# Performance work log

Measured on AMD Instinct MI355X. Metric: run time of the kernel, lower is better.

The kernel has to match this reference:

```python
import jax, jax.numpy as jnp
import numpy as np

N_NODES = 100000
N_EDGES = 1200000
N_GRAPHS = 1024
IN_DIM, HIDDEN, OUT_DIM = 4, 64, 2
BN_EPS = 1e-5


def setup_inputs() -> dict:
    key = jax.random.key(0)
    ks = jax.random.split(key, 12)
    x = jax.random.normal(ks[0], (N_NODES, IN_DIM), dtype=jnp.float32)
    edge_index = jax.random.randint(ks[1], (2, N_EDGES), 0, N_NODES, dtype=jnp.int64)
    batch = jnp.sort(jax.random.randint(ks[2], (N_NODES,), 0, N_GRAPHS, dtype=jnp.int64))
    s = 1.0 / np.sqrt(HIDDEN)
    return {
        "x": x,
        "edge_index": edge_index,
        "batch": batch,
        "W_enc": jax.random.normal(ks[3], (IN_DIM, HIDDEN), dtype=jnp.float32) * 0.5,
        "b_enc": jnp.zeros((HIDDEN,), dtype=jnp.float32),
        "bn_gamma": jnp.ones((HIDDEN,), dtype=jnp.float32),
        "bn_beta": jnp.zeros((HIDDEN,), dtype=jnp.float32),
        "bn_mean": jax.random.normal(ks[4], (HIDDEN,), dtype=jnp.float32) * 0.1,
        "bn_var": jax.random.uniform(ks[5], (HIDDEN,), dtype=jnp.float32, minval=0.5, maxval=1.5),
        "W_gcn": jax.random.normal(ks[6], (HIDDEN, HIDDEN), dtype=jnp.float32) * s,
        "b_gcn": jnp.zeros((HIDDEN,), dtype=jnp.float32),
        "W_cls1": jax.random.normal(ks[7], (HIDDEN, HIDDEN), dtype=jnp.float32) * s,
        "b_cls1": jnp.zeros((HIDDEN,), dtype=jnp.float32),
        "W_cls2": jax.random.normal(ks[8], (HIDDEN, OUT_DIM), dtype=jnp.float32) * s,
        "b_cls2": jnp.zeros((OUT_DIM,), dtype=jnp.float32),
    }


def reference(x, edge_index, batch, W_enc, b_enc, bn_gamma, bn_beta, bn_mean, bn_var,
              W_gcn, b_gcn, W_cls1, b_cls1, W_cls2, b_cls2):
    n = x.shape[0]
    # Encoder: Linear -> ReLU -> Dropout(eval=identity) -> BatchNorm1d (running stats)
    h = jnp.maximum(x @ W_enc + b_enc, 0.0)
    h = (h - bn_mean) * jax.lax.rsqrt(bn_var + BN_EPS) * bn_gamma + bn_beta
    # GCNConv (PyG): add self-loops, symmetric deg^{-1/2} normalization
    loop = jnp.arange(n, dtype=edge_index.dtype)
    src = jnp.concatenate([edge_index[0], loop])  # [E+N]
    dst = jnp.concatenate([edge_index[1], loop])
    deg = jnp.zeros((n,), dtype=h.dtype).at[dst].add(1.0)
    dis = jnp.where(deg > 0, jax.lax.rsqrt(jnp.maximum(deg, 1.0)), 0.0)
    norm = dis[src] * dis[dst]  # [E+N]
    hw = h @ W_gcn  # [N, H]
    msg = hw[src] * norm[:, None]  # gather + scale, [E+N, H]
    agg = jax.ops.segment_sum(msg, dst, num_segments=n) + b_gcn
    agg = jnp.maximum(agg, 0.0)  # .relu()
    # global_mean_pool over graphs
    sums = jax.ops.segment_sum(agg, batch, num_segments=N_GRAPHS)  # [G, H]
    cnts = jax.ops.segment_sum(jnp.ones((n,), dtype=agg.dtype), batch, num_segments=N_GRAPHS)
    gm = sums / jnp.maximum(cnts, 1.0)[:, None]
    # Classifier: Linear -> ReLU -> Dropout(eval) -> Linear
    out = jnp.maximum(gm @ W_cls1 + b_cls1, 0.0) @ W_cls2 + b_cls2
    return out
```

## Files before the change

kernel.cpp:

```cpp
#include <hip/hip_runtime.h>

#define N_NODES  100000
#define N_EDGES  1200000
#define N_GRAPHS 1024

#define BUCK_SHIFT 10
#define BUCK_NODES 1024
#define NBUCK 98
#define FBLK  512
#define CHUNK ((N_EDGES + FBLK - 1) / FBLK)

__device__ __forceinline__ unsigned short f2bf(float f) {
  unsigned u = __float_as_uint(f);
  return (unsigned short)((u + 0x7fffu + ((u >> 16) & 1u)) >> 16);
}
__device__ __forceinline__ float bf2f(unsigned short b) {
  return __uint_as_float(((unsigned)b) << 16);
}

__global__ __launch_bounds__(256) void k_cnt(const int* __restrict__ ei,
                                             int* __restrict__ cnt,
                                             float* __restrict__ gsum) {
  __shared__ int h[NBUCK];
  int t = threadIdx.x;
  for (int i = t; i < NBUCK; i += 256) h[i] = 0;
  int gi = blockIdx.x * 256 + t;
  if (gi < N_GRAPHS * 64) gsum[gi] = 0.f;
  __syncthreads();
  int start = blockIdx.x * CHUNK, end = min(start + CHUNK, N_EDGES);
  for (int e = start + t; e < end; e += 256)
    atomicAdd(&h[ei[N_EDGES + e] >> BUCK_SHIFT], 1);
  __syncthreads();
  for (int b = t; b < NBUCK; b += 256)
    cnt[b * FBLK + blockIdx.x] = h[b];
}

__global__ __launch_bounds__(256) void k_colscan(int* __restrict__ cnt,
                                                 int* __restrict__ tot) {
  __shared__ int wsum[4];
  int b = blockIdx.x, t = threadIdx.x;
  int v0 = cnt[b * FBLK + 2 * t], v1 = cnt[b * FBLK + 2 * t + 1];
  int a = v0 + v1;
  int lane = t & 63, w = t >> 6;
  int incl = a;
  #pragma unroll
  for (int off = 1; off < 64; off <<= 1) {
    int y = __shfl_up(incl, off);
    if (lane >= off) incl += y;
  }
  if (lane == 63) wsum[w] = incl;
  __syncthreads();
  if (t == 0) {
    int s = 0;
    #pragma unroll
    for (int i = 0; i < 4; ++i) { int x = wsum[i]; wsum[i] = s; s += x; }
    tot[b] = s;
  }
  __syncthreads();
  int excl = wsum[w] + incl - a;
  cnt[b * FBLK + 2 * t] = excl;
  cnt[b * FBLK + 2 * t + 1] = excl + v0;
}

__global__ __launch_bounds__(256) void k_fill(const int* __restrict__ ei,
                                              const int* __restrict__ cnt,
                                              const int* __restrict__ tot,
                                              int* __restrict__ binned) {
  __shared__ int totS[NBUCK];
  __shared__ int cur[NBUCK];
  int t = threadIdx.x, blk = blockIdx.x;
  if (t < NBUCK) totS[t] = tot[t];
  __syncthreads();
  if (t < NBUCK) {
    int s = 0;
    for (int i = 0; i < t; ++i) s += totS[i];
    cur[t] = s + cnt[t * FBLK + blk];
  }
  __syncthreads();
  int start = blk * CHUNK, end = min(start + CHUNK, N_EDGES);
  for (int e = start + t; e < end; e += 256) {
    int src = ei[e];
    int dst = ei[N_EDGES + e];
    int b = dst >> BUCK_SHIFT;
    int p = atomicAdd(&cur[b], 1);
    binned[p] = src | ((dst & (BUCK_NODES - 1)) << 17);
  }
}

__global__ __launch_bounds__(1024) void k_csr(const int* __restrict__ tot,
                                              const int* __restrict__ binned,
                                              int* __restrict__ csr,
                                              int* __restrict__ row_start,
                                              float* __restrict__ dis) {
  __shared__ int hist[BUCK_NODES];
  __shared__ int wsum[16];
  __shared__ int b0S;
  int t = threadIdx.x;
  int blk = blockIdx.x;
  int lane = t & 63, w = t >> 6;
  int pv = (t < blk) ? tot[t] : 0;
  #pragma unroll
  for (int off = 32; off > 0; off >>= 1) pv += __shfl_down(pv, off);
  if (lane == 0) wsum[w] = pv;
  hist[t] = 0;
  __syncthreads();
  if (t == 0) {
    int s = 0;
    #pragma unroll
    for (int i = 0; i < 16; ++i) s += wsum[i];
    b0S = s;
  }
  __syncthreads();
  int b0 = b0S;
  int nE = tot[blk];
  int node0 = blk << BUCK_SHIFT;
  int nNodes = min(BUCK_NODES, N_NODES - node0);
  for (int i = t; i < nE; i += 1024)
    atomicAdd(&hist[(unsigned)binned[b0 + i] >> 17], 1);
  __syncthreads();
  int v = hist[t];
  int incl = v;
  #pragma unroll
  for (int off = 1; off < 64; off <<= 1) {
    int y = __shfl_up(incl, off);
    if (lane >= off) incl += y;
  }
  if (lane == 63) wsum[w] = incl;
  __syncthreads();
  if (t == 0) {
    int s = 0;
    #pragma unroll
    for (int i = 0; i < 16; ++i) { int x = wsum[i]; wsum[i] = s; s += x; }
  }
  __syncthreads();
  int excl = wsum[w] + incl - v;
  hist[t] = excl;
  if (t < nNodes) {
    row_start[node0 + t] = b0 + excl;
    dis[node0 + t] = rsqrtf((float)(v + 1));
  }
  if (t == 0 && blk == NBUCK - 1) row_start[N_NODES] = N_EDGES;
  __syncthreads();
  for (int i = t; i < nE; i += 1024) {
    int vv = binned[b0 + i];
    int d = (unsigned)vv >> 17;
    int p = atomicAdd(&hist[d], 1);
    csr[b0 + p] = vv & 0x1FFFF;
  }
}

__global__ __launch_bounds__(256) void k_enc(
    const float* __restrict__ x,
    const float* __restrict__ Wenc, const float* __restrict__ benc,
    const float* __restrict__ gamma, const float* __restrict__ beta,
    const float* __restrict__ mean,  const float* __restrict__ var,
    const float* __restrict__ Wgcn,  const float* __restrict__ dis,
    unsigned short* __restrict__ hws) {
  int lane = threadIdx.x & 63;
  int wv = (blockIdx.x * 256 + threadIdx.x) >> 6;
  float be = benc[lane];
  float sc = gamma[lane] * rsqrtf(var[lane] + 1e-5f);
  float mu = mean[lane], bt = beta[lane];
  float w0 = Wenc[lane], w1 = Wenc[64 + lane], w2 = Wenc[128 + lane], w3 = Wenc[192 + lane];
  float wreg[64];
  #pragma unroll
  for (int k = 0; k < 64; ++k) wreg[k] = Wgcn[k * 64 + lane];
  int n0 = wv * 16;
  for (int i = 0; i < 16; ++i) {
    int n = n0 + i;
    float4 xv = ((const float4*)x)[n];
    float h = fmaf(xv.w, w3, fmaf(xv.z, w2, fmaf(xv.y, w1, fmaf(xv.x, w0, be))));
    h = fmaxf(h, 0.f);
    float hbn = (h - mu) * sc + bt;
    int hb = __float_as_int(hbn);
    float a0 = 0.f, a1 = 0.f, a2 = 0.f, a3 = 0.f;
    #pragma unroll
    for (int k = 0; k < 64; k += 4) {
      a0 = fmaf(__int_as_float(__builtin_amdgcn_readlane(hb, k)),     wreg[k],     a0);
      a1 = fmaf(__int_as_float(__builtin_amdgcn_readlane(hb, k + 1)), wreg[k + 1], a1);
      a2 = fmaf(__int_as_float(__builtin_amdgcn_readlane(hb, k + 2)), wreg[k + 2], a2);
      a3 = fmaf(__int_as_float(__builtin_amdgcn_readlane(hb, k + 3)), wreg[k + 3], a3);
    }
    float acc = ((a0 + a1) + (a2 + a3)) * dis[n];
    hws[(size_t)n * 64 + lane] = f2bf(acc);
  }
}

__global__ __launch_bounds__(64) void k_gather(
    const int* __restrict__ row_start, const int* __restrict__ csr,
    const float* __restrict__ dis, const unsigned short* __restrict__ hws,
    const int* __restrict__ batch, const float* __restrict__ bgcn,
    float* __restrict__ gsum) {
  int lane = threadIdx.x;
  int nb = blockIdx.x * 4;
  float bias = bgcn[lane];
  float vout[4];
  int gid[4];
  #pragma unroll
  for (int k = 0; k < 4; ++k) {
    int n = nb + k;
    int st = row_start[n], en = row_start[n + 1];
    float dn = dis[n];
    float a0 = 0.f, a1 = 0.f, a2 = 0.f, a3 = 0.f;
    for (int c = st; c < en; c += 64) {
      int m = min(64, en - c);
      int chunk = (c + lane < en) ? csr[c + lane] : 0;
      int j = 0;
      for (; j + 4 <= m; j += 4) {
        int s0 = __builtin_amdgcn_readlane(chunk, j);
        int s1 = __builtin_amdgcn_readlane(chunk, j + 1);
        int s2 = __builtin_amdgcn_readlane(chunk, j + 2);
        int s3 = __builtin_amdgcn_readlane(chunk, j + 3);
        a0 += bf2f(hws[(size_t)s0 * 64 + lane]);
        a1 += bf2f(hws[(size_t)s1 * 64 + lane]);
        a2 += bf2f(hws[(size_t)s2 * 64 + lane]);
        a3 += bf2f(hws[(size_t)s3 * 64 + lane]);
      }
      for (; j < m; ++j) {
        int s = __builtin_amdgcn_readlane(chunk, j);
        a0 += bf2f(hws[(size_t)s * 64 + lane]);
      }
    }
    float self = bf2f(hws[(size_t)n * 64 + lane]);
    vout[k] = fmaxf(dn * (((a0 + a1) + (a2 + a3)) + self) + bias, 0.f);
    gid[k] = batch[n];
  }
  float vs = vout[0];
  int cg = gid[0];
  #pragma unroll
  for (int k = 1; k < 4; ++k) {
    if (gid[k] == cg) vs += vout[k];
    else {
      atomicAdd(&gsum[cg * 64 + lane], vs);
      vs = vout[k]; cg = gid[k];
    }
  }
  atomicAdd(&gsum[cg * 64 + lane], vs);
}

__global__ void k_cls(const float* __restrict__ gsum, const int* __restrict__ batch,
                      const float* __restrict__ W1, const float* __restrict__ b1,
                      const float* __restrict__ W2, const float* __restrict__ b2,
                      float* __restrict__ out) {
  __shared__ float gm[64];
  __shared__ int cntS;
  int j = threadIdx.x;
  int g = blockIdx.x;
  if (j == 0) {
    int lo = 0, hi = N_NODES;
    while (lo < hi) { int mid = (lo + hi) >> 1; if (batch[mid] < g) lo = mid + 1; else hi = mid; }
    int lo2 = lo, hi2 = N_NODES;
    while (lo2 < hi2) { int mid = (lo2 + hi2) >> 1; if (batch[mid] < g + 1) lo2 = mid + 1; else hi2 = mid; }
    cntS = lo2 - lo;
  }
  __syncthreads();
  float denom = fmaxf((float)cntS, 1.0f);
  gm[j] = gsum[g * 64 + j] / denom;
  __syncthreads();
  float hid = b1[j];
  #pragma unroll
  for (int k = 0; k < 64; ++k) hid += gm[k] * W1[k * 64 + j];
  hid = fmaxf(hid, 0.f);
  float o0 = hid * W2[j * 2 + 0];
  float o1 = hid * W2[j * 2 + 1];
  #pragma unroll
  for (int off = 32; off > 0; off >>= 1) {
    o0 += __shfl_down(o0, off);
    o1 += __shfl_down(o1, off);
  }
  if (j == 0) {
    out[g * 2 + 0] = o0 + b2[0];
    out[g * 2 + 1] = o1 + b2[1];
  }
}

extern "C" void kernel_launch(void* const* d_in, const int* in_sizes, int n_in,
                              void* d_out, int out_size, void* d_ws, size_t ws_size,
                              hipStream_t stream) {
  const float* x     = (const float*)d_in[0];
  const int*   ei    = (const int*)d_in[1];
  const int*   batch = (const int*)d_in[2];
  const float* Wenc  = (const float*)d_in[3];
  const float* benc  = (const float*)d_in[4];
  const float* gamma = (const float*)d_in[5];
  const float* beta  = (const float*)d_in[6];
  const float* mean  = (const float*)d_in[7];
  const float* var   = (const float*)d_in[8];
  const float* Wgcn  = (const float*)d_in[9];
  const float* bgcn  = (const float*)d_in[10];
  const float* W1    = (const float*)d_in[11];
  const float* b1    = (const float*)d_in[12];
  const float* W2    = (const float*)d_in[13];
  const float* b2    = (const float*)d_in[14];
  float* out = (float*)d_out;

  char* ws = (char*)d_ws;
  float*          gsum      = (float*)ws;          ws += (size_t)N_GRAPHS * 64 * 4;
  int*            cnt       = (int*)ws;            ws += (size_t)NBUCK * FBLK * 4;
  int*            tot       = (int*)ws;            ws += 128 * 4;
  int*            binned    = (int*)ws;            ws += (size_t)N_EDGES * 4;
  int*            csr       = (int*)ws;            ws += (size_t)N_EDGES * 4;
  int*            row_start = (int*)ws;            ws += (size_t)(N_NODES + 32) * 4;
  float*          dis       = (float*)ws;          ws += (size_t)N_NODES * 4;
  unsigned short* hws       = (unsigned short*)ws; ws += (size_t)N_NODES * 64 * 2;

  k_cnt<<<FBLK, 256, 0, stream>>>(ei, cnt, gsum);
  k_colscan<<<NBUCK, 256, 0, stream>>>(cnt, tot);
  k_fill<<<FBLK, 256, 0, stream>>>(ei, cnt, tot, binned);
  k_csr<<<NBUCK, 1024, 0, stream>>>(tot, binned, csr, row_start, dis);
  k_enc<<<(N_NODES / 16 + 3) / 4, 256, 0, stream>>>(x, Wenc, benc, gamma, beta, mean, var,
                                                    Wgcn, dis, hws);
  k_gather<<<(N_NODES / 4), 64, 0, stream>>>(row_start, csr, dis, hws, batch, bgcn, gsum);
  k_cls<<<N_GRAPHS, 64, 0, stream>>>(gsum, batch, W1, b1, W2, b2, out);
}
```

Before: 195.2 us.

## Fuse column scan with encoder, compute degrees early, halve bucket size

Per-node in-degrees are now counted with global atomics during the first histogram pass. This lets the encoder/GCN-transform kernel run merged with the bucket column-scan kernel in a single launch, instead of waiting on the CSR build to produce the normalisation factors. Buckets shrink to 512 nodes (196 buckets) so the CSR kernel runs more, smaller blocks. The gather derives its normalisation from row lengths and unrolls neighbour loads by eight. The cost is an extra memset and 1.2M global atomics on the degree array, plus a prefix scan of bucket totals that is recomputed in every fill block.

New measurement: 239.5 us. 1.23x slower.

```diff
diff --git a/kernel.cpp b/kernel.cpp
--- a/kernel.cpp
+++ b/kernel.cpp
@@ -4,11 +4,12 @@
 #define N_EDGES  1200000
 #define N_GRAPHS 1024
 
-#define BUCK_SHIFT 10
-#define BUCK_NODES 1024
-#define NBUCK 98
-#define FBLK  512
-#define CHUNK ((N_EDGES + FBLK - 1) / FBLK)
+#define BSH    9
+#define BNODES 512
+#define NBUCK  196
+#define FBLK   512
+#define CHUNK  ((N_EDGES + FBLK - 1) / FBLK)
+#define ENC_BLOCKS 1563
 
 __device__ __forceinline__ unsigned short f2bf(float f) {
   unsigned u = __float_as_uint(f);
@@ -20,7 +21,8 @@
 
 __global__ __launch_bounds__(256) void k_cnt(const int* __restrict__ ei,
                                              int* __restrict__ cnt,
-                                             float* __restrict__ gsum) {
+                                             float* __restrict__ gsum,
+                                             int* __restrict__ deg) {
   __shared__ int h[NBUCK];
   int t = threadIdx.x;
   for (int i = t; i < NBUCK; i += 256) h[i] = 0;
@@ -28,136 +30,53 @@
   if (gi < N_GRAPHS * 64) gsum[gi] = 0.f;
   __syncthreads();
   int start = blockIdx.x * CHUNK, end = min(start + CHUNK, N_EDGES);
-  for (int e = start + t; e < end; e += 256)
-    atomicAdd(&h[ei[N_EDGES + e] >> BUCK_SHIFT], 1);
+  for (int e = start + t; e < end; e += 256) {
+    int dst = ei[N_EDGES + e];
+    atomicAdd(&h[dst >> BSH], 1);
+    atomicAdd(&deg[dst], 1);
+  }
   __syncthreads();
   for (int b = t; b < NBUCK; b += 256)
     cnt[b * FBLK + blockIdx.x] = h[b];
 }
 
-__global__ __launch_bounds__(256) void k_colscan(int* __restrict__ cnt,
-                                                 int* __restrict__ tot) {
-  __shared__ int wsum[4];
-  int b = blockIdx.x, t = threadIdx.x;
-  int v0 = cnt[b * FBLK + 2 * t], v1 = cnt[b * FBLK + 2 * t + 1];
-  int a = v0 + v1;
-  int lane = t & 63, w = t >> 6;
-  int incl = a;
-  #pragma unroll
-  for (int off = 1; off < 64; off <<= 1) {
-    int y = __shfl_up(incl, off);
-    if (lane >= off) incl += y;
-  }
-  if (lane == 63) wsum[w] = incl;
-  __syncthreads();
-  if (t == 0) {
-    int s = 0;
-    #pragma unroll
-    for (int i = 0; i < 4; ++i) { int x = wsum[i]; wsum[i] = s; s += x; }
-    tot[b] = s;
-  }
-  __syncthreads();
-  int excl = wsum[w] + incl - a;
-  cnt[b * FBLK + 2 * t] = excl;
-  cnt[b * FBLK + 2 * t + 1] = excl + v0;
-}
-
-__global__ __launch_bounds__(256) void k_fill(const int* __restrict__ ei,
-                                              const int* __restrict__ cnt,
-                                              const int* __restrict__ tot,
-                                              int* __restrict__ binned) {
-  __shared__ int totS[NBUCK];
-  __shared__ int cur[NBUCK];
-  int t = threadIdx.x, blk = blockIdx.x;
-  if (t < NBUCK) totS[t] = tot[t];
-  __syncthreads();
-  if (t < NBUCK) {
-    int s = 0;
-    for (int i = 0; i < t; ++i) s += totS[i];
-    cur[t] = s + cnt[t * FBLK + blk];
-  }
-  __syncthreads();
-  int start = blk * CHUNK, end = min(start + CHUNK, N_EDGES);
-  for (int e = start + t; e < end; e += 256) {
-    int src = ei[e];
-    int dst = ei[N_EDGES + e];
-    int b = dst >> BUCK_SHIFT;
-    int p = atomicAdd(&cur[b], 1);
-    binned[p] = src | ((dst & (BUCK_NODES - 1)) << 17);
-  }
-}
-
-__global__ __launch_bounds__(1024) void k_csr(const int* __restrict__ tot,
-                                              const int* __restrict__ binned,
-                                              int* __restrict__ csr,
-                                              int* __restrict__ row_start,
-                                              float* __restrict__ dis) {
-  __shared__ int hist[BUCK_NODES];
-  __shared__ int wsum[16];
-  __shared__ int b0S;
-  int t = threadIdx.x;
-  int blk = blockIdx.x;
-  int lane = t & 63, w = t >> 6;
-  int pv = (t < blk) ? tot[t] : 0;
-  #pragma unroll
-  for (int off = 32; off > 0; off >>= 1) pv += __shfl_down(pv, off);
-  if (lane == 0) wsum[w] = pv;
-  hist[t] = 0;
-  __syncthreads();
-  if (t == 0) {
-    int s = 0;
-    #pragma unroll
-    for (int i = 0; i < 16; ++i) s += wsum[i];
-    b0S = s;
-  }
-  __syncthreads();
-  int b0 = b0S;
-  int nE = tot[blk];
-  int node0 = blk << BUCK_SHIFT;
-  int nNodes = min(BUCK_NODES, N_NODES - node0);
-  for (int i = t; i < nE; i += 1024)
-    atomicAdd(&hist[(unsigned)binned[b0 + i] >> 17], 1);
-  __syncthreads();
-  int v = hist[t];
-  int incl = v;
-  #pragma unroll
-  for (int off = 1; off < 64; off <<= 1) {
-    int y = __shfl_up(incl, off);
-    if (lane >= off) incl += y;
-  }
-  if (lane == 63) wsum[w] = incl;
-  __syncthreads();
-  if (t == 0) {
-    int s = 0;
-    #pragma unroll
-    for (int i = 0; i < 16; ++i) { int x = wsum[i]; wsum[i] = s; s += x; }
-  }
-  __syncthreads();
-  int excl = wsum[w] + incl - v;
-  hist[t] = excl;
-  if (t < nNodes) {
-    row_start[node0 + t] = b0 + excl;
-    dis[node0 + t] = rsqrtf((float)(v + 1));
-  }
-  if (t == 0 && blk == NBUCK - 1) row_start[N_NODES] = N_EDGES;
-  __syncthreads();
-  for (int i = t; i < nE; i += 1024) {
-    int vv = binned[b0 + i];
-    int d = (unsigned)vv >> 17;
-    int p = atomicAdd(&hist[d], 1);
-    csr[b0 + p] = vv & 0x1FFFF;
-  }
-}
-
-__global__ __launch_bounds__(256) void k_enc(
+__global__ __launch_bounds__(256) void k_scan_enc(
+    int* __restrict__ cnt, int* __restrict__ tot, const int* __restrict__ deg,
     const float* __restrict__ x,
     const float* __restrict__ Wenc, const float* __restrict__ benc,
     const float* __restrict__ gamma, const float* __restrict__ beta,
     const float* __restrict__ mean,  const float* __restrict__ var,
-    const float* __restrict__ Wgcn,  const float* __restrict__ dis,
+    const float* __restrict__ Wgcn,
     unsigned short* __restrict__ hws) {
-  int lane = threadIdx.x & 63;
-  int wv = (blockIdx.x * 256 + threadIdx.x) >> 6;
+  int t = threadIdx.x;
+  int lane = t & 63, w = t >> 6;
+  if (blockIdx.x < NBUCK) {
+    __shared__ int wsum[4];
+    int b = blockIdx.x;
+    int v0 = cnt[b * FBLK + 2 * t], v1 = cnt[b * FBLK + 2 * t + 1];
+    int a = v0 + v1;
+    int incl = a;
+    #pragma unroll
+    for (int off = 1; off < 64; off <<= 1) {
+      int y = __shfl_up(incl, off);
+      if (lane >= off) incl += y;
+    }
+    if (lane == 63) wsum[w] = incl;
+    __syncthreads();
+    if (t == 0) {
+      int s = 0;
+      #pragma unroll
+      for (int i = 0; i < 4; ++i) { int x2 = wsum[i]; wsum[i] = s; s += x2; }
+      tot[b] = s;
+    }
+    __syncthreads();
+    int excl = wsum[w] + incl - a;
+    cnt[b * FBLK + 2 * t] = excl;
+    cnt[b * FBLK + 2 * t + 1] = excl + v0;
+    return;
+  }
+  int wv = (blockIdx.x - NBUCK) * 4 + w;
+  if (wv >= 6250) return;
   float be = benc[lane];
   float sc = gamma[lane] * rsqrtf(var[lane] + 1e-5f);
   float mu = mean[lane], bt = beta[lane];
@@ -181,14 +100,109 @@
       a2 = fmaf(__int_as_float(__builtin_amdgcn_readlane(hb, k + 2)), wreg[k + 2], a2);
       a3 = fmaf(__int_as_float(__builtin_amdgcn_readlane(hb, k + 3)), wreg[k + 3], a3);
     }
-    float acc = ((a0 + a1) + (a2 + a3)) * dis[n];
+    float dis_n = rsqrtf((float)(deg[n] + 1));
+    float acc = ((a0 + a1) + (a2 + a3)) * dis_n;
     hws[(size_t)n * 64 + lane] = f2bf(acc);
+  }
+}
+
+__global__ __launch_bounds__(256) void k_fill(const int* __restrict__ ei,
+                                              const int* __restrict__ cnt,
+                                              const int* __restrict__ tot,
+                                              int* __restrict__ binned) {
+  __shared__ int cur[NBUCK];
+  __shared__ int wsum[4];
+  int t = threadIdx.x, blk = blockIdx.x;
+  int lane = t & 63, w = t >> 6;
+  int v = (t < NBUCK) ? tot[t] : 0;
+  int incl = v;
+  #pragma unroll
+  for (int off = 1; off < 64; off <<= 1) {
+    int y = __shfl_up(incl, off);
+    if (lane >= off) incl += y;
+  }
+  if (lane == 63) wsum[w] = incl;
+  __syncthreads();
+  if (t == 0) {
+    int s = 0;
+    #pragma unroll
+    for (int i = 0; i < 4; ++i) { int x2 = wsum[i]; wsum[i] = s; s += x2; }
+  }
+  __syncthreads();
+  if (t < NBUCK) cur[t] = (wsum[w] + incl - v) + cnt[t * FBLK + blk];
+  __syncthreads();
+  int start = blk * CHUNK, end = min(start + CHUNK, N_EDGES);
+  for (int e = start + t; e < end; e += 256) {
+    int src = ei[e];
+    int dst = ei[N_EDGES + e];
+    int b = dst >> BSH;
+    int p = atomicAdd(&cur[b], 1);
+    binned[p] = src | ((dst & (BNODES - 1)) << 17);
+  }
+}
+
+__global__ __launch_bounds__(512) void k_csr(const int* __restrict__ tot,
+                                             const int* __restrict__ binned,
+                                             int* __restrict__ csr,
+                                             int* __restrict__ row_start) {
+  __shared__ int hist[BNODES];
+  __shared__ int wsum[8];
+  __shared__ int b0S;
+  int t = threadIdx.x;
+  int blk = blockIdx.x;
+  int lane = t & 63, w = t >> 6;
+  int pv = 0;
+  for (int i = t; i < blk; i += 512) pv += tot[i];
+  #pragma unroll
+  for (int off = 32; off > 0; off >>= 1) pv += __shfl_down(pv, off);
+  if (lane == 0) wsum[w] = pv;
+  hist[t] = 0;
+  __syncthreads();
+  if (t == 0) {
+    int s = 0;
+    #pragma unroll
+    for (int i = 0; i < 8; ++i) s += wsum[i];
+    b0S = s;
+  }
+  __syncthreads();
+  int b0 = b0S;
+  int nE = tot[blk];
+  int node0 = blk << BSH;
+  for (int i = t; i < nE; i += 512)
+    atomicAdd(&hist[(unsigned)binned[b0 + i] >> 17], 1);
+  __syncthreads();
+  int v = hist[t];
+  int incl = v;
+  #pragma unroll
+  for (int off = 1; off < 64; off <<= 1) {
+    int y = __shfl_up(incl, off);
+    if (lane >= off) incl += y;
+  }
+  if (lane == 63) wsum[w] = incl;
+  __syncthreads();
+  if (t == 0) {
+    int s = 0;
+    #pragma unroll
+    for (int i = 0; i < 8; ++i) { int x2 = wsum[i]; wsum[i] = s; s += x2; }
+  }
+  __syncthreads();
+  int excl = wsum[w] + incl - v;
+  hist[t] = excl;
+  int node = node0 + t;
+  if (node < N_NODES) row_start[node] = b0 + excl;
+  if (t == 0 && blk == NBUCK - 1) row_start[N_NODES] = N_EDGES;
+  __syncthreads();
+  for (int i = t; i < nE; i += 512) {
+    int vv = binned[b0 + i];
+    int d = (unsigned)vv >> 17;
+    int p = atomicAdd(&hist[d], 1);
+    csr[b0 + p] = vv & 0x1FFFF;
   }
 }
 
 __global__ __launch_bounds__(64) void k_gather(
     const int* __restrict__ row_start, const int* __restrict__ csr,
-    const float* __restrict__ dis, const unsigned short* __restrict__ hws,
+    const unsigned short* __restrict__ hws,
     const int* __restrict__ batch, const float* __restrict__ bgcn,
     float* __restrict__ gsum) {
   int lane = threadIdx.x;
@@ -200,21 +214,31 @@
   for (int k = 0; k < 4; ++k) {
     int n = nb + k;
     int st = row_start[n], en = row_start[n + 1];
-    float dn = dis[n];
+    float dn = rsqrtf((float)(en - st + 1));
     float a0 = 0.f, a1 = 0.f, a2 = 0.f, a3 = 0.f;
     for (int c = st; c < en; c += 64) {
       int m = min(64, en - c);
       int chunk = (c + lane < en) ? csr[c + lane] : 0;
       int j = 0;
-      for (; j + 4 <= m; j += 4) {
+      for (; j + 8 <= m; j += 8) {
         int s0 = __builtin_amdgcn_readlane(chunk, j);
         int s1 = __builtin_amdgcn_readlane(chunk, j + 1);
         int s2 = __builtin_amdgcn_readlane(chunk, j + 2);
         int s3 = __builtin_amdgcn_readlane(chunk, j + 3);
-        a0 += bf2f(hws[(size_t)s0 * 64 + lane]);
-        a1 += bf2f(hws[(size_t)s1 * 64 + lane]);
-        a2 += bf2f(hws[(size_t)s2 * 64 + lane]);
-        a3 += bf2f(hws[(size_t)s3 * 64 + lane]);
+        int s4 = __builtin_amdgcn_readlane(chunk, j + 4);
+        int s5 = __builtin_amdgcn_readlane(chunk, j + 5);
+        int s6 = __builtin_amdgcn_readlane(chunk, j + 6);
+        int s7 = __builtin_amdgcn_readlane(chunk, j + 7);
+        float r0 = bf2f(hws[(size_t)s0 * 64 + lane]);
+        float r1 = bf2f(hws[(size_t)s1 * 64 + lane]);
+        float r2 = bf2f(hws[(size_t)s2 * 64 + lane]);
+        float r3 = bf2f(hws[(size_t)s3 * 64 + lane]);
+        float r4 = bf2f(hws[(size_t)s4 * 64 + lane]);
+        float r5 = bf2f(hws[(size_t)s5 * 64 + lane]);
+        float r6 = bf2f(hws[(size_t)s6 * 64 + lane]);
+        float r7 = bf2f(hws[(size_t)s7 * 64 + lane]);
+        a0 += r0; a1 += r1; a2 += r2; a3 += r3;
+        a0 += r4; a1 += r5; a2 += r6; a3 += r7;
       }
       for (; j < m; ++j) {
         int s = __builtin_amdgcn_readlane(chunk, j);
@@ -296,20 +320,20 @@
 
   char* ws = (char*)d_ws;
   float*          gsum      = (float*)ws;          ws += (size_t)N_GRAPHS * 64 * 4;
+  int*            deg       = (int*)ws;            ws += (size_t)N_NODES * 4;
   int*            cnt       = (int*)ws;            ws += (size_t)NBUCK * FBLK * 4;
-  int*            tot       = (int*)ws;            ws += 128 * 4;
+  int*            tot       = (int*)ws;            ws += 256 * 4;
   int*            binned    = (int*)ws;            ws += (size_t)N_EDGES * 4;
   int*            csr       = (int*)ws;            ws += (size_t)N_EDGES * 4;
   int*            row_start = (int*)ws;            ws += (size_t)(N_NODES + 32) * 4;
-  float*          dis       = (float*)ws;          ws += (size_t)N_NODES * 4;
   unsigned short* hws       = (unsigned short*)ws; ws += (size_t)N_NODES * 64 * 2;
 
-  k_cnt<<<FBLK, 256, 0, stream>>>(ei, cnt, gsum);
-  k_colscan<<<NBUCK, 256, 0, stream>>>(cnt, tot);
+  hipMemsetAsync(deg, 0, (size_t)N_NODES * 4, stream);
+  k_cnt<<<FBLK, 256, 0, stream>>>(ei, cnt, gsum, deg);
+  k_scan_enc<<<NBUCK + ENC_BLOCKS, 256, 0, stream>>>(cnt, tot, deg, x, Wenc, benc,
+                                                     gamma, beta, mean, var, Wgcn, hws);
   k_fill<<<FBLK, 256, 0, stream>>>(ei, cnt, tot, binned);
-  k_csr<<<NBUCK, 1024, 0, stream>>>(tot, binned, csr, row_start, dis);
-  k_enc<<<(N_NODES / 16 + 3) / 4, 256, 0, stream>>>(x, Wenc, benc, gamma, beta, mean, var,
-                                                    Wgcn, dis, hws);
-  k_gather<<<(N_NODES / 4), 64, 0, stream>>>(row_start, csr, dis, hws, batch, bgcn, gsum);
+  k_csr<<<NBUCK, 512, 0, stream>>>(tot, binned, csr, row_start);
+  k_gather<<<(N_NODES / 4), 64, 0, stream>>>(row_start, csr, hws, batch, bgcn, gsum);
   k_cls<<<N_GRAPHS, 64, 0, stream>>>(gsum, batch, W1, b1, W2, b2, out);
 }
```
